# Kernel tuning notes

Measured on AMD Instinct MI355X. Metric: run time of the kernel, lower is better.

Reference implementation:

```python
import jax, jax.numpy as jnp
import numpy as np

SIGMA = 1.0
EPSILON = 1.0
MAX_ITER = 10


def pairwise_kernel(x, y, sigma=SIGMA):
    # k = -||x-y||^2 / (2 sigma^2), shape [B, L, K]
    outer = jnp.einsum('bld,bkd->blk', x, y)
    nx = jnp.sum(x * x, axis=2)
    ny = jnp.sum(y * y, axis=2)
    dist = jnp.clip(nx[:, :, None] + ny[:, None, :] - 2.0 * outer, 0.0, None)
    return -dist / (2.0 * sigma ** 2)


def c_transform(potential, log_weight, kernel, epsilon=EPSILON):
    # rho=None => scale=1, lse = -eps * logsumexp(kernel/eps + (pot/eps + log_w))
    s = potential / epsilon + log_weight            # [B, K]
    operand = kernel / epsilon + s[:, None, :]      # [B, L, K]
    return -epsilon * jax.scipy.special.logsumexp(operand, axis=2)


def potentials(kxy, log_a, log_b):
    kyx = jnp.swapaxes(kxy, 1, 2)
    f0 = jnp.zeros_like(log_a)
    g0 = jnp.zeros_like(log_b)

    def step(carry, _):
        f, g = carry
        fn = c_transform(g, log_b, kxy)
        gn = c_transform(f, log_a, kyx)
        return ((fn + f) * 0.5, (gn + g) * 0.5), None

    (f, g), _ = jax.lax.scan(step, (f0, g0), None, length=MAX_ITER)
    return f, g


def sym_potential(x, log_a):
    kxx = pairwise_kernel(x, x)
    f0 = jnp.zeros_like(log_a)

    def step(f, _):
        fn = c_transform(f, log_a, kxx)
        return (fn + f) * 0.5, None

    f, _ = jax.lax.scan(step, f0, None, length=MAX_ITER)
    return f


def evaluate_potential(x, a, y, b, g):
    # phi_transform is identity for rho=None; scaled_dot_prod forward = sum(a*f, dim=1)
    kxy = pairwise_kernel(x, y)
    f = c_transform(g, jnp.log(b), kxy)
    return jnp.sum(a * f, axis=1)


def setup_inputs() -> dict:
    key = jax.random.key(0)
    k1, k2, k3, k4 = jax.random.split(key, 4)
    B, L, K, D = 8, 2048, 2048, 32
    x = jax.random.normal(k1, (B, L, D), dtype=jnp.float32)
    y = jax.random.normal(k2, (B, K, D), dtype=jnp.float32)
    a = jax.random.uniform(k3, (B, L), dtype=jnp.float32, minval=0.1, maxval=1.0)
    b = jax.random.uniform(k4, (B, K), dtype=jnp.float32, minval=0.1, maxval=1.0)
    a = a / jnp.sum(a, axis=1, keepdims=True)
    b = b / jnp.sum(b, axis=1, keepdims=True)
    return {"x": x, "a": a, "y": y, "b": b}


def reference(x, a, y, b):
    log_a, log_b = jnp.log(a), jnp.log(b)
    kxy = pairwise_kernel(x, y)
    f, g = potentials(kxy, log_a, log_b)
    dist = evaluate_potential(x, a, y, b, g) + evaluate_potential(y, b, x, a, f)
    fx = sym_potential(x, log_a)
    fy = sym_potential(y, log_b)
    ent_x = evaluate_potential(x, a, x, a, fx)
    ent_y = evaluate_potential(y, b, y, b, fy)
    return jnp.mean(dist - ent_x - ent_y)
```

## Files before the change

### kernel.cpp

```cpp
#include <hip/hip_runtime.h>
#include <math.h>

#define BATCH 8
#define NPT   2048
#define DIM   32
#define RPB   64
#define STRIPS (RPB / 16)
#define NBLKR (NPT / RPB)
#define CPW   (NPT / 4)
#define NT    (CPW / 16)
#define L2E   1.44269504088896f
#define LN2   0.6931471805599453f
#define BN    (BATCH * NPT)

typedef __attribute__((ext_vector_type(8))) _Float16 half8;
typedef __attribute__((ext_vector_type(4))) float floatx4;
typedef unsigned short u16;
typedef unsigned int u32;

__device__ __forceinline__ u16 f2h_bits(float v) {
    _Float16 h = (_Float16)v;
    return *(u16*)&h;
}
__device__ __forceinline__ float exp2v(float x) { return __builtin_amdgcn_exp2f(x); }

struct SymSet {
    const u16* Ah;
    const u16* Bh;
    const float* tls;
    const float* qX;
    const float* bmIn;
    const float* cwNext;
    const float* prev;
    float* out;
    float* tlsOut;
    float* bmOut;
};
struct FusedSet {
    const u16* Xh;
    const u16* Ysh;
    const float* tlsG;
    const float* tlsF;
    const float* qX;
    const float* bmG;
    const float* bmF;
    const float* c_x;
    const float* prevF;
    float* outF;
    float* tlsFOut;
    float* bmFOut;
    float* gpart;
};
struct CtArgs { FusedSet fs; SymSet s[2]; int average; };

__global__ __launch_bounds__(256, 3) void ct2_kernel(CtArgs args) {
    const int batch = blockIdx.z;
    const int row0 = blockIdx.x * RPB;
    const int tid  = threadIdx.x;
    const int w = tid >> 6, lane = tid & 63, n = lane & 15, quad = lane >> 4;
    const int qk = quad * 8;
    const size_t pbase = (size_t)batch * NPT * DIM;
    const size_t vbase = (size_t)batch * NPT;

    __shared__ float lsum[RPB][4];

    if (blockIdx.y == 0) {
        const FusedSet fs = args.fs;
        const u16* __restrict__ Ah = fs.Xh + pbase;
        const u16* __restrict__ Bh = fs.Ysh + pbase;
        const float* __restrict__ tg = fs.tlsG + vbase;
        const float* __restrict__ tf = fs.tlsF + vbase;

        half8 ah[STRIPS];
        #pragma unroll
        for (int s = 0; s < STRIPS; s++) {
            size_t off = (size_t)(row0 + s * 16 + n) * DIM + qk;
            ah[s] = *(const half8*)(Ah + off);
        }

        float mg = fmaxf(fs.bmG[batch * 128 + lane], fs.bmG[batch * 128 + 64 + lane]);
        float mf = fmaxf(fs.bmF[batch * 128 + lane], fs.bmF[batch * 128 + 64 + lane]);
        #pragma unroll
        for (int m = 1; m < 64; m <<= 1) {
            mg = fmaxf(mg, __shfl_xor(mg, m, 64));
            mf = fmaxf(mf, __shfl_xor(mf, m, 64));
        }
        const float TmaxG = mg;
        const float l2eTG = L2E * mg, l2eTF = L2E * mf;

        floatx4 cis[STRIPS];
        #pragma unroll
        for (int s = 0; s < STRIPS; s++)
            #pragma unroll
            for (int r = 0; r < 4; r++)
                cis[s][r] = tf[row0 + s * 16 + quad * 4 + r] - l2eTF;

        float sumF[STRIPS][4];
        #pragma unroll
        for (int s = 0; s < STRIPS; s++)
            #pragma unroll
            for (int r = 0; r < 4; r++) sumF[s][r] = 0.0f;

        const int c0 = w * CPW + n;
        const u16* bp = Bh + (size_t)c0 * DIM + qk;
        const float* tp = tg + c0;
        float* gpc = fs.gpart + ((size_t)batch * NBLKR + blockIdx.x) * NPT + c0;

        half8 bb[4];
        float tt[4];
        bb[0] = *(const half8*)bp;                       tt[0] = tp[0];
        bb[1] = *(const half8*)(bp + (size_t)16 * DIM);  tt[1] = tp[16];

        auto tile = [&](half8 b, float t, int idx) {
            float wq = exp2v(t - l2eTG);
            floatx4 acc[STRIPS];
            #pragma unroll
            for (int s = 0; s < STRIPS; s++)
                acc[s] = __builtin_amdgcn_mfma_f32_16x16x32_f16(ah[s], b, cis[s], 0, 0, 0);
            float gl = 0.0f;
            #pragma unroll
            for (int s = 0; s < STRIPS; s++)
                #pragma unroll
                for (int r = 0; r < 4; r++) {
                    float e = exp2v(acc[s][r]);
                    sumF[s][r] = fmaf(wq, e, sumF[s][r]);
                    gl += e;
                }
            gl += __shfl_xor(gl, 16, 64);
            gl += __shfl_xor(gl, 32, 64);
            if (lane < 16) gpc[idx * 16] = gl;
        };

        #pragma unroll 1
        for (int ch = 0; ch < NT; ch += 4) {
            #pragma unroll
            for (int j = 0; j < 4; j++) {
                int nx = ch + j + 2;
                int nxc = nx < NT ? nx : NT - 1;
                bb[(j + 2) & 3] = *(const half8*)(bp + (size_t)nxc * 16 * DIM);
                tt[(j + 2) & 3] = tp[nxc * 16];
                tile(bb[j], tt[j], ch + j);
            }
        }

        #pragma unroll
        for (int s = 0; s < STRIPS; s++)
            #pragma unroll
            for (int r = 0; r < 4; r++) {
                float v = sumF[s][r];
                #pragma unroll
                for (int m = 1; m < 16; m <<= 1) v += __shfl_xor(v, m, 64);
                if (n == 0) lsum[s * 16 + quad * 4 + r][w] = v;
            }
        __syncthreads();

        if (tid < RPB) {
            float T = (lsum[tid][0] + lsum[tid][1]) + (lsum[tid][2] + lsum[tid][3]);
            int l = row0 + tid;
            float lse = TmaxG + __logf(T) - LN2 * (tf[l] - l2eTF);
            float val = fs.qX[vbase + l] - lse;
            if (args.average) val = 0.5f * (fs.prevF[vbase + l] + val);
            fs.outF[vbase + l] = val;
            float tc = val + fs.c_x[vbase + l];
            fs.tlsFOut[vbase + l] = L2E * tc;
            float bm = tc;
            #pragma unroll
            for (int m = 1; m < 16; m <<= 1) bm = fmaxf(bm, __shfl_xor(bm, m, 64));
            if ((tid & 15) == 0)
                fs.bmFOut[batch * 128 + blockIdx.x * STRIPS + (tid >> 4)] = bm;
        }
    } else {
        const SymSet cs = args.s[blockIdx.y - 1];
        const u16* __restrict__ Ah = cs.Ah + pbase;
        const u16* __restrict__ Bh = cs.Bh + pbase;
        const float* __restrict__ tls = cs.tls + vbase;

        half8 ah[STRIPS];
        #pragma unroll
        for (int s = 0; s < STRIPS; s++) {
            size_t off = (size_t)(row0 + s * 16 + n) * DIM + qk;
            ah[s] = *(const half8*)(Ah + off);
        }

        float tmv = fmaxf(cs.bmIn[batch * 128 + lane], cs.bmIn[batch * 128 + 64 + lane]);
        #pragma unroll
        for (int m = 1; m < 64; m <<= 1) tmv = fmaxf(tmv, __shfl_xor(tmv, m, 64));
        const float Tmax = tmv;
        const float l2eTmax = L2E * Tmax;

        float sum[STRIPS][4];
        #pragma unroll
        for (int s = 0; s < STRIPS; s++)
            #pragma unroll
            for (int r = 0; r < 4; r++) sum[s][r] = 0.0f;

        const int c0 = w * CPW + n;
        const u16* bp = Bh + (size_t)c0 * DIM + qk;
        const float* tp = tls + c0;

        half8 bb[4];
        float tt[4];
        bb[0] = *(const half8*)bp;                       tt[0] = tp[0];
        bb[1] = *(const half8*)(bp + (size_t)16 * DIM);  tt[1] = tp[16];

        auto tile = [&](half8 b, float t) {
            float bias = t - l2eTmax;
            floatx4 ci = (floatx4){bias, bias, bias, bias};
            floatx4 acc[STRIPS];
            #pragma unroll
            for (int s = 0; s < STRIPS; s++)
                acc[s] = __builtin_amdgcn_mfma_f32_16x16x32_f16(ah[s], b, ci, 0, 0, 0);
            #pragma unroll
            for (int s = 0; s < STRIPS; s++)
                #pragma unroll
                for (int r = 0; r < 4; r++)
                    sum[s][r] += exp2v(acc[s][r]);
        };

        #pragma unroll 1
        for (int ch = 0; ch < NT; ch += 4) {
            #pragma unroll
            for (int j = 0; j < 4; j++) {
                int nx = ch + j + 2;
                int nxc = nx < NT ? nx : NT - 1;
                bb[(j + 2) & 3] = *(const half8*)(bp + (size_t)nxc * 16 * DIM);
                tt[(j + 2) & 3] = tp[nxc * 16];
                tile(bb[j], tt[j]);
            }
        }

        #pragma unroll
        for (int s = 0; s < STRIPS; s++)
            #pragma unroll
            for (int r = 0; r < 4; r++) {
                float v = sum[s][r];
                #pragma unroll
                for (int m = 1; m < 16; m <<= 1) v += __shfl_xor(v, m, 64);
                if (n == 0) lsum[s * 16 + quad * 4 + r][w] = v;
            }
        __syncthreads();

        if (tid < RPB) {
            float T = (lsum[tid][0] + lsum[tid][1]) + (lsum[tid][2] + lsum[tid][3]);
            int l = row0 + tid;
            float lse = Tmax + __logf(T);
            float val = cs.qX[vbase + l] - lse;
            if (args.average) val = 0.5f * (cs.prev[vbase + l] + val);
            cs.out[vbase + l] = val;
            float tc = val + cs.cwNext[vbase + l];
            cs.tlsOut[vbase + l] = L2E * tc;
            float bm = tc;
            #pragma unroll
            for (int m = 1; m < 16; m <<= 1) bm = fmaxf(bm, __shfl_xor(bm, m, 64));
            if ((tid & 15) == 0)
                cs.bmOut[batch * 128 + blockIdx.x * STRIPS + (tid >> 4)] = bm;
        }
    }
}

struct GfArgs {
    const float* gpart;
    const float* bmF;
    const float* qY;
    const float* prevG;
    const float* c_y;
    float* outG;
    float* tlsGOut;
    float* bmGOut;
    int average;
};

__global__ __launch_bounds__(256) void gfin_kernel(GfArgs a) {
    const int tid = threadIdx.x;
    const int batch = blockIdx.x >> 5;
    const int chunk = blockIdx.x & 31;
    const int g = tid >> 6, c = tid & 63;
    const int col = chunk * 64 + c;

    __shared__ float sb[128];
    __shared__ float ps[4][64];
    if (tid < 128) sb[tid] = a.bmF[batch * 128 + tid];
    __syncthreads();

    float m = fmaxf(sb[tid & 63], sb[(tid & 63) + 64]);
    #pragma unroll
    for (int k = 1; k < 64; k <<= 1) m = fmaxf(m, __shfl_xor(m, k, 64));
    const float Tmax = m;

    const float* gp = a.gpart + ((size_t)batch * NBLKR + g) * NPT + col;
    float G = 0.0f;
    #pragma unroll
    for (int p = 0; p < NBLKR / 4; p++) G += gp[(size_t)p * 4 * NPT];
    ps[g][c] = G;
    __syncthreads();

    if (tid < 64) {
        float Gt = (ps[0][tid] + ps[1][tid]) + (ps[2][tid] + ps[3][tid]);
        const int colT = chunk * 64 + tid;
        const size_t idx = (size_t)batch * NPT + colT;
        float val = a.qY[idx] - (Tmax + __logf(Gt));
        if (a.average) val = 0.5f * (a.prevG[idx] + val);
        a.outG[idx] = val;
        float tc = val + a.c_y[idx];
        a.tlsGOut[idx] = L2E * tc;
        float bm = tc;
        #pragma unroll
        for (int k = 1; k < 16; k <<= 1) bm = fmaxf(bm, __shfl_xor(bm, k, 64));
        if ((tid & 15) == 0) a.bmGOut[batch * 128 + (colT >> 4)] = bm;
    }
}

struct InitArgs {
    const float *x, *a, *y, *b;
    float *c_x, *c_y, *qx, *qy;
    u16 *xh, *yh, *xsh, *ysh;
    float *f0, *g0, *fx0, *fy0;
    float *tlsF0, *tlsG0, *tlsFx0, *tlsFy0;
    float *bmF0, *bmG0, *bmFx0, *bmFy0;
};

__global__ __launch_bounds__(256) void init_kernel(InitArgs ia) {
    int idx = blockIdx.x * 256 + threadIdx.x;
    if (idx >= BN) return;
    const float* xp = ia.x + (size_t)idx * DIM;
    const float* yp = ia.y + (size_t)idx * DIM;
    u32* xhp  = (u32*)ia.xh  + (size_t)idx * (DIM / 2);
    u32* yhp  = (u32*)ia.yh  + (size_t)idx * (DIM / 2);
    u32* xshp = (u32*)ia.xsh + (size_t)idx * (DIM / 2);
    u32* yshp = (u32*)ia.ysh + (size_t)idx * (DIM / 2);
    float sx = 0.f, sy = 0.f;
    #pragma unroll
    for (int d = 0; d < DIM; d += 2) {
        float v0 = xp[d], v1 = xp[d + 1];
        sx += v0 * v0 + v1 * v1;
        xhp[d / 2]  = (u32)f2h_bits(v0) | ((u32)f2h_bits(v1) << 16);
        xshp[d / 2] = (u32)f2h_bits(L2E * v0) | ((u32)f2h_bits(L2E * v1) << 16);
        float u0 = yp[d], u1 = yp[d + 1];
        sy += u0 * u0 + u1 * u1;
        yhp[d / 2]  = (u32)f2h_bits(u0) | ((u32)f2h_bits(u1) << 16);
        yshp[d / 2] = (u32)f2h_bits(L2E * u0) | ((u32)f2h_bits(L2E * u1) << 16);
    }
    float qxv = 0.5f * sx, qyv = 0.5f * sy;
    ia.qx[idx] = qxv; ia.qy[idx] = qyv;
    float cxv = __logf(ia.a[idx]) - qxv;
    float cyv = __logf(ia.b[idx]) - qyv;
    ia.c_x[idx] = cxv; ia.c_y[idx] = cyv;
    ia.f0[idx] = 0.f; ia.g0[idx] = 0.f; ia.fx0[idx] = 0.f; ia.fy0[idx] = 0.f;
    ia.tlsF0[idx] = L2E * cxv; ia.tlsG0[idx] = L2E * cyv;
    ia.tlsFx0[idx] = L2E * cxv; ia.tlsFy0[idx] = L2E * cyv;
    float mx = cxv, my = cyv;
    #pragma unroll
    for (int m = 1; m < 16; m <<= 1) {
        mx = fmaxf(mx, __shfl_xor(mx, m, 32));
        my = fmaxf(my, __shfl_xor(my, m, 32));
    }
    if ((threadIdx.x & 15) == 0) {
        int g = idx >> 4;
        ia.bmF0[g] = mx; ia.bmFx0[g] = mx;
        ia.bmG0[g] = my; ia.bmFy0[g] = my;
    }
}

__global__ __launch_bounds__(1024) void reduce_kernel(
        const float* __restrict__ a, const float* __restrict__ b,
        const float* __restrict__ ctA, const float* __restrict__ ctB,
        const float* __restrict__ ctX, const float* __restrict__ ctY,
        float* __restrict__ out) {
    float acc = 0.f;
    for (int idx = threadIdx.x; idx < BN; idx += 1024) {
        acc += a[idx] * (ctA[idx] - ctX[idx]) + b[idx] * (ctB[idx] - ctY[idx]);
    }
    #pragma unroll
    for (int off = 32; off > 0; off >>= 1) acc += __shfl_down(acc, off, 64);
    __shared__ float sm[16];
    if ((threadIdx.x & 63) == 0) sm[threadIdx.x >> 6] = acc;
    __syncthreads();
    if (threadIdx.x == 0) {
        float t = 0.f;
        #pragma unroll
        for (int i = 0; i < 16; i++) t += sm[i];
        out[0] = t / (float)BATCH;
    }
}

extern "C" void kernel_launch(void* const* d_in, const int* in_sizes, int n_in,
                              void* d_out, int out_size, void* d_ws, size_t ws_size,
                              hipStream_t stream) {
    const float* x = (const float*)d_in[0];
    const float* a = (const float*)d_in[1];
    const float* y = (const float*)d_in[2];
    const float* b = (const float*)d_in[3];
    float* out = (float*)d_out;

    float* ws = (float*)d_ws;
    float* c_x = ws + 0 * BN;
    float* c_y = ws + 1 * BN;
    float* qx  = ws + 2 * BN;
    float* qy  = ws + 3 * BN;
    float* fb[2]  = { ws + 4 * BN,  ws + 5 * BN };
    float* gb[2]  = { ws + 6 * BN,  ws + 7 * BN };
    float* fxb[2] = { ws + 8 * BN,  ws + 9 * BN };
    float* fyb[2] = { ws + 10 * BN, ws + 11 * BN };
    float* ctA = ws + 12 * BN;
    float* ctB = ws + 13 * BN;
    float* ctX = ws + 14 * BN;
    float* ctY = ws + 15 * BN;
    float* tlsF[2]  = { ws + 16 * BN, ws + 17 * BN };
    float* tlsG[2]  = { ws + 18 * BN, ws + 19 * BN };
    float* tlsFx[2] = { ws + 20 * BN, ws + 21 * BN };
    float* tlsFy[2] = { ws + 22 * BN, ws + 23 * BN };
    float* dummyT = ws + 24 * BN;
    float* small = ws + 25 * BN;
    float* bmF[2]  = { small + 0 * 1024, small + 1 * 1024 };
    float* bmG[2]  = { small + 2 * 1024, small + 3 * 1024 };
    float* bmFx[2] = { small + 4 * 1024, small + 5 * 1024 };
    float* bmFy[2] = { small + 6 * 1024, small + 7 * 1024 };
    float* dummyB = small + 8 * 1024;
    u16* bf = (u16*)(small + 10 * 1024);
    const size_t AS = (size_t)BN * DIM;
    u16* xh  = bf + 0 * AS;
    u16* yh  = bf + 1 * AS;
    u16* xsh = bf + 2 * AS;
    u16* ysh = bf + 3 * AS;
    float* gpart = (float*)(bf + 4 * AS);

    InitArgs ia;
    ia.x = x; ia.a = a; ia.y = y; ia.b = b;
    ia.c_x = c_x; ia.c_y = c_y; ia.qx = qx; ia.qy = qy;
    ia.xh = xh; ia.yh = yh; ia.xsh = xsh; ia.ysh = ysh;
    ia.f0 = fb[0]; ia.g0 = gb[0]; ia.fx0 = fxb[0]; ia.fy0 = fyb[0];
    ia.tlsF0 = tlsF[0]; ia.tlsG0 = tlsG[0]; ia.tlsFx0 = tlsFx[0]; ia.tlsFy0 = tlsFy[0];
    ia.bmF0 = bmF[0]; ia.bmG0 = bmG[0]; ia.bmFx0 = bmFx[0]; ia.bmFy0 = bmFy[0];
    init_kernel<<<BN / 256, 256, 0, stream>>>(ia);

    dim3 grid(NBLKR, 3, BATCH);
    int cur = 0;
    for (int it = 0; it < 10; it++) {
        CtArgs ar;
        ar.average = 1;
        ar.fs = { xh, ysh, tlsG[cur], tlsF[cur], qx, bmG[cur], bmF[cur], c_x,
                  fb[cur], fb[1 - cur], tlsF[1 - cur], bmF[1 - cur], gpart };
        ar.s[0] = { xh, xsh, tlsFx[cur], qx, bmFx[cur], c_x,
                    fxb[cur], fxb[1 - cur], tlsFx[1 - cur], bmFx[1 - cur] };
        ar.s[1] = { yh, ysh, tlsFy[cur], qy, bmFy[cur], c_y,
                    fyb[cur], fyb[1 - cur], tlsFy[1 - cur], bmFy[1 - cur] };
        ct2_kernel<<<grid, 256, 0, stream>>>(ar);

        GfArgs ga = { gpart, bmF[cur], qy, gb[cur], c_y,
                      gb[1 - cur], tlsG[1 - cur], bmG[1 - cur], 1 };
        gfin_kernel<<<256, 256, 0, stream>>>(ga);
        cur ^= 1;
    }

    CtArgs fin;
    fin.average = 0;
    fin.fs = { xh, ysh, tlsG[cur], tlsF[cur], qx, bmG[cur], bmF[cur], c_x,
               fb[cur], ctA, dummyT, dummyB, gpart };
    fin.s[0] = { xh, xsh, tlsFx[cur], qx, bmFx[cur], c_x, fxb[cur], ctX, dummyT, dummyB };
    fin.s[1] = { yh, ysh, tlsFy[cur], qy, bmFy[cur], c_y, fyb[cur], ctY, dummyT, dummyB };
    ct2_kernel<<<grid, 256, 0, stream>>>(fin);

    GfArgs gf = { gpart, bmF[cur], qy, gb[cur], c_y, ctB, dummyT, dummyB, 0 };
    gfin_kernel<<<256, 256, 0, stream>>>(gf);

    reduce_kernel<<<1, 1024, 0, stream>>>(a, b, ctA, ctB, ctX, ctY, out);
}
```

Before: 325.0 us.

## Halve rows per block, double occupancy, and shorten B-operand prefetch pipeline

Rows per block drop from 64 to 32 (two MFMA strips instead of four) and the launch bound asks for six blocks per CU instead of three, so more waves are resident to hide latency. The 4-deep rotating prefetch buffer becomes a 2-deep ping-pong with a conditional load, which cuts register use. The per-tile column sum becomes an explicit tree add. Halving RPB doubles the number of blocks and the gpart partial rows, and each B tile is reused across fewer rows, so global/L2 traffic for B rises.

```diff
diff --git a/kernel.cpp b/kernel.cpp
--- a/kernel.cpp
+++ b/kernel.cpp
@@ -4,7 +4,7 @@
 #define BATCH 8
 #define NPT   2048
 #define DIM   32
-#define RPB   64
+#define RPB   32
 #define STRIPS (RPB / 16)
 #define NBLKR (NPT / RPB)
 #define CPW   (NPT / 4)
@@ -53,7 +53,7 @@
 };
 struct CtArgs { FusedSet fs; SymSet s[2]; int average; };
 
-__global__ __launch_bounds__(256, 3) void ct2_kernel(CtArgs args) {
+__global__ __launch_bounds__(256, 6) void ct2_kernel(CtArgs args) {
     const int batch = blockIdx.z;
     const int row0 = blockIdx.x * RPB;
     const int tid  = threadIdx.x;
@@ -106,10 +106,9 @@
         const float* tp = tg + c0;
         float* gpc = fs.gpart + ((size_t)batch * NBLKR + blockIdx.x) * NPT + c0;
 
-        half8 bb[4];
-        float tt[4];
-        bb[0] = *(const half8*)bp;                       tt[0] = tp[0];
-        bb[1] = *(const half8*)(bp + (size_t)16 * DIM);  tt[1] = tp[16];
+        half8 b0, b1;
+        float t0, t1;
+        b0 = *(const half8*)bp;  t0 = *tp;
 
         auto tile = [&](half8 b, float t, int idx) {
             float wq = exp2v(t - l2eTG);
@@ -117,30 +116,31 @@
             #pragma unroll
             for (int s = 0; s < STRIPS; s++)
                 acc[s] = __builtin_amdgcn_mfma_f32_16x16x32_f16(ah[s], b, cis[s], 0, 0, 0);
-            float gl = 0.0f;
+            float e[STRIPS][4];
             #pragma unroll
             for (int s = 0; s < STRIPS; s++)
                 #pragma unroll
                 for (int r = 0; r < 4; r++) {
-                    float e = exp2v(acc[s][r]);
-                    sumF[s][r] = fmaf(wq, e, sumF[s][r]);
-                    gl += e;
+                    e[s][r] = exp2v(acc[s][r]);
+                    sumF[s][r] = fmaf(wq, e[s][r], sumF[s][r]);
                 }
+            float gl = ((e[0][0] + e[0][1]) + (e[0][2] + e[0][3]))
+                     + ((e[1][0] + e[1][1]) + (e[1][2] + e[1][3]));
             gl += __shfl_xor(gl, 16, 64);
             gl += __shfl_xor(gl, 32, 64);
             if (lane < 16) gpc[idx * 16] = gl;
         };
 
         #pragma unroll 1
-        for (int ch = 0; ch < NT; ch += 4) {
-            #pragma unroll
-            for (int j = 0; j < 4; j++) {
-                int nx = ch + j + 2;
-                int nxc = nx < NT ? nx : NT - 1;
-                bb[(j + 2) & 3] = *(const half8*)(bp + (size_t)nxc * 16 * DIM);
-                tt[(j + 2) & 3] = tp[nxc * 16];
-                tile(bb[j], tt[j], ch + j);
+        for (int ch = 0; ch < NT; ch += 2) {
+            b1 = *(const half8*)(bp + (size_t)(ch + 1) * 16 * DIM);
+            t1 = tp[(ch + 1) * 16];
+            tile(b0, t0, ch);
+            if (ch + 2 < NT) {
+                b0 = *(const half8*)(bp + (size_t)(ch + 2) * 16 * DIM);
+                t0 = tp[(ch + 2) * 16];
             }
+            tile(b1, t1, ch + 1);
         }
 
         #pragma unroll
@@ -198,10 +198,9 @@
         const u16* bp = Bh + (size_t)c0 * DIM + qk;
         const float* tp = tls + c0;
 
-        half8 bb[4];
-        float tt[4];
-        bb[0] = *(const half8*)bp;                       tt[0] = tp[0];
-        bb[1] = *(const half8*)(bp + (size_t)16 * DIM);  tt[1] = tp[16];
+        half8 b0, b1;
+        float t0, t1;
+        b0 = *(const half8*)bp;  t0 = *tp;
 
         auto tile = [&](half8 b, float t) {
             float bias = t - l2eTmax;
@@ -218,15 +217,15 @@
         };
 
         #pragma unroll 1
-        for (int ch = 0; ch < NT; ch += 4) {
-            #pragma unroll
-            for (int j = 0; j < 4; j++) {
-                int nx = ch + j + 2;
-                int nxc = nx < NT ? nx : NT - 1;
-                bb[(j + 2) & 3] = *(const half8*)(bp + (size_t)nxc * 16 * DIM);
-                tt[(j + 2) & 3] = tp[nxc * 16];
-                tile(bb[j], tt[j]);
+        for (int ch = 0; ch < NT; ch += 2) {
+            b1 = *(const half8*)(bp + (size_t)(ch + 1) * 16 * DIM);
+            t1 = tp[(ch + 1) * 16];
+            tile(b0, t0);
+            if (ch + 2 < NT) {
+                b0 = *(const half8*)(bp + (size_t)(ch + 2) * 16 * DIM);
+                t0 = tp[(ch + 2) * 16];
             }
+            tile(b1, t1);
         }
 
         #pragma unroll
```

Result: slower. 369.0 us (+13.5%).

## Fold g-potential finalization into next c-transform kernel and fuse final reduction

Applied to the files above, without the earlier changes.

Removes the separate gfin kernel per iteration. Each fused c-transform block now reduces the previous iteration's column partial sums itself, computes the averaged g potential, its max and log-weights into shared memory, and then runs the f update. The final g-transform and the scalar reduction are merged into one kernel that uses an atomic add. This cuts about ten kernel launches and the global round trips for tlsG and bmG. In exchange every block redundantly sums 32 partial rows for all 2048 columns, and a double-buffered gpart array plus extra shared memory and syncs are added.

```diff
diff --git a/kernel.cpp b/kernel.cpp
--- a/kernel.cpp
+++ b/kernel.cpp
@@ -39,23 +39,30 @@
 struct FusedSet {
     const u16* Xh;
     const u16* Ysh;
-    const float* tlsG;
     const float* tlsF;
     const float* qX;
-    const float* bmG;
     const float* bmF;
     const float* c_x;
     const float* prevF;
     float* outF;
     float* tlsFOut;
     float* bmFOut;
-    float* gpart;
+    const float* gpIn;
+    float* gpOut;
+    const float* gbIn;
+    float* gbOut;
+    const float* stfIn;
+    float* stfOut;
+    const float* qY;
+    const float* c_y;
+    int first;
 };
 struct CtArgs { FusedSet fs; SymSet s[2]; int average; };
 
-__global__ __launch_bounds__(256, 3) void ct2_kernel(CtArgs args) {
+__global__ __launch_bounds__(256, 3) void ct3_kernel(CtArgs args) {
     const int batch = blockIdx.z;
-    const int row0 = blockIdx.x * RPB;
+    const int xb = blockIdx.x;
+    const int row0 = xb * RPB;
     const int tid  = threadIdx.x;
     const int w = tid >> 6, lane = tid & 63, n = lane & 15, quad = lane >> 4;
     const int qk = quad * 8;
@@ -63,13 +70,56 @@
     const size_t vbase = (size_t)batch * NPT;
 
     __shared__ float lsum[RPB][4];
+    __shared__ float sg[NPT];
 
     if (blockIdx.y == 0) {
         const FusedSet fs = args.fs;
         const u16* __restrict__ Ah = fs.Xh + pbase;
         const u16* __restrict__ Bh = fs.Ysh + pbase;
-        const float* __restrict__ tg = fs.tlsG + vbase;
         const float* __restrict__ tf = fs.tlsF + vbase;
+        const float* __restrict__ qYp = fs.qY + vbase;
+        const float* __restrict__ cyp = fs.c_y + vbase;
+        const float* __restrict__ gbInp = fs.gbIn + vbase;
+        float* gbOutp = fs.gbOut + vbase;
+
+        float tcv[8];
+        float lmax = -1e30f;
+        if (!fs.first) {
+            const float mfPrev = fs.stfIn[0];
+            const float* gpi = fs.gpIn + (size_t)batch * NBLKR * NPT;
+            #pragma unroll
+            for (int j = 0; j < 8; j++) {
+                const int col = tid + j * 256;
+                float G = 0.f;
+                #pragma unroll 8
+                for (int p = 0; p < NBLKR; p++) G += gpi[(size_t)p * NPT + col];
+                float raw = qYp[col] - (mfPrev + __logf(G));
+                float gnew = 0.5f * (gbInp[col] + raw);
+                if (xb == 0) gbOutp[col] = gnew;
+                float tc = gnew + cyp[col];
+                tcv[j] = tc;
+                lmax = fmaxf(lmax, tc);
+            }
+        } else {
+            #pragma unroll
+            for (int j = 0; j < 8; j++) {
+                const int col = tid + j * 256;
+                if (xb == 0) gbOutp[col] = 0.f;
+                float tc = cyp[col];
+                tcv[j] = tc;
+                lmax = fmaxf(lmax, tc);
+            }
+        }
+        #pragma unroll
+        for (int m = 1; m < 64; m <<= 1) lmax = fmaxf(lmax, __shfl_xor(lmax, m, 64));
+        if (lane == 0) lsum[0][w] = lmax;
+        __syncthreads();
+        const float TmaxG = fmaxf(fmaxf(lsum[0][0], lsum[0][1]),
+                                  fmaxf(lsum[0][2], lsum[0][3]));
+        #pragma unroll
+        for (int j = 0; j < 8; j++)
+            sg[tid + j * 256] = L2E * (tcv[j] - TmaxG);
+        __syncthreads();
 
         half8 ah[STRIPS];
         #pragma unroll
@@ -77,16 +127,11 @@
             size_t off = (size_t)(row0 + s * 16 + n) * DIM + qk;
             ah[s] = *(const half8*)(Ah + off);
         }
-
-        float mg = fmaxf(fs.bmG[batch * 128 + lane], fs.bmG[batch * 128 + 64 + lane]);
         float mf = fmaxf(fs.bmF[batch * 128 + lane], fs.bmF[batch * 128 + 64 + lane]);
         #pragma unroll
-        for (int m = 1; m < 64; m <<= 1) {
-            mg = fmaxf(mg, __shfl_xor(mg, m, 64));
-            mf = fmaxf(mf, __shfl_xor(mf, m, 64));
-        }
-        const float TmaxG = mg;
-        const float l2eTG = L2E * mg, l2eTF = L2E * mf;
+        for (int m = 1; m < 64; m <<= 1) mf = fmaxf(mf, __shfl_xor(mf, m, 64));
+        const float l2eTF = L2E * mf;
+        if (xb == 0 && tid == 0) fs.stfOut[0] = mf;
 
         floatx4 cis[STRIPS];
         #pragma unroll
@@ -103,16 +148,14 @@
 
         const int c0 = w * CPW + n;
         const u16* bp = Bh + (size_t)c0 * DIM + qk;
-        const float* tp = tg + c0;
-        float* gpc = fs.gpart + ((size_t)batch * NBLKR + blockIdx.x) * NPT + c0;
+        float* gpc = fs.gpOut + ((size_t)batch * NBLKR + xb) * NPT + c0;
 
         half8 bb[4];
-        float tt[4];
-        bb[0] = *(const half8*)bp;                       tt[0] = tp[0];
-        bb[1] = *(const half8*)(bp + (size_t)16 * DIM);  tt[1] = tp[16];
-
-        auto tile = [&](half8 b, float t, int idx) {
-            float wq = exp2v(t - l2eTG);
+        bb[0] = *(const half8*)bp;
+        bb[1] = *(const half8*)(bp + (size_t)16 * DIM);
+
+        auto tile = [&](half8 b, int idx) {
+            float wq = exp2v(sg[c0 + idx * 16]);
             floatx4 acc[STRIPS];
             #pragma unroll
             for (int s = 0; s < STRIPS; s++)
@@ -138,8 +181,7 @@
                 int nx = ch + j + 2;
                 int nxc = nx < NT ? nx : NT - 1;
                 bb[(j + 2) & 3] = *(const half8*)(bp + (size_t)nxc * 16 * DIM);
-                tt[(j + 2) & 3] = tp[nxc * 16];
-                tile(bb[j], tt[j], ch + j);
+                tile(bb[j], ch + j);
             }
         }
 
@@ -167,7 +209,7 @@
             #pragma unroll
             for (int m = 1; m < 16; m <<= 1) bm = fmaxf(bm, __shfl_xor(bm, m, 64));
             if ((tid & 15) == 0)
-                fs.bmFOut[batch * 128 + blockIdx.x * STRIPS + (tid >> 4)] = bm;
+                fs.bmFOut[batch * 128 + xb * STRIPS + (tid >> 4)] = bm;
         }
     } else {
         const SymSet cs = args.s[blockIdx.y - 1];
@@ -253,41 +295,34 @@
             #pragma unroll
             for (int m = 1; m < 16; m <<= 1) bm = fmaxf(bm, __shfl_xor(bm, m, 64));
             if ((tid & 15) == 0)
-                cs.bmOut[batch * 128 + blockIdx.x * STRIPS + (tid >> 4)] = bm;
+                cs.bmOut[batch * 128 + xb * STRIPS + (tid >> 4)] = bm;
         }
     }
 }
 
-struct GfArgs {
+struct FrArgs {
     const float* gpart;
-    const float* bmF;
+    const float* stf;
     const float* qY;
-    const float* prevG;
-    const float* c_y;
-    float* outG;
-    float* tlsGOut;
-    float* bmGOut;
-    int average;
+    const float* a;
+    const float* b;
+    const float* ctA;
+    const float* ctX;
+    const float* ctY;
+    float* out;
 };
 
-__global__ __launch_bounds__(256) void gfin_kernel(GfArgs a) {
+__global__ __launch_bounds__(256) void finredux_kernel(FrArgs fa) {
     const int tid = threadIdx.x;
     const int batch = blockIdx.x >> 5;
     const int chunk = blockIdx.x & 31;
     const int g = tid >> 6, c = tid & 63;
     const int col = chunk * 64 + c;
 
-    __shared__ float sb[128];
     __shared__ float ps[4][64];
-    if (tid < 128) sb[tid] = a.bmF[batch * 128 + tid];
-    __syncthreads();
-
-    float m = fmaxf(sb[tid & 63], sb[(tid & 63) + 64]);
-    #pragma unroll
-    for (int k = 1; k < 64; k <<= 1) m = fmaxf(m, __shfl_xor(m, k, 64));
-    const float Tmax = m;
-
-    const float* gp = a.gpart + ((size_t)batch * NBLKR + g) * NPT + col;
+    const float mf = fa.stf[0];
+
+    const float* gp = fa.gpart + ((size_t)batch * NBLKR + g) * NPT + col;
     float G = 0.0f;
     #pragma unroll
     for (int p = 0; p < NBLKR / 4; p++) G += gp[(size_t)p * 4 * NPT];
@@ -298,15 +333,12 @@
         float Gt = (ps[0][tid] + ps[1][tid]) + (ps[2][tid] + ps[3][tid]);
         const int colT = chunk * 64 + tid;
         const size_t idx = (size_t)batch * NPT + colT;
-        float val = a.qY[idx] - (Tmax + __logf(Gt));
-        if (a.average) val = 0.5f * (a.prevG[idx] + val);
-        a.outG[idx] = val;
-        float tc = val + a.c_y[idx];
-        a.tlsGOut[idx] = L2E * tc;
-        float bm = tc;
-        #pragma unroll
-        for (int k = 1; k < 16; k <<= 1) bm = fmaxf(bm, __shfl_xor(bm, k, 64));
-        if ((tid & 15) == 0) a.bmGOut[batch * 128 + (colT >> 4)] = bm;
+        float ctB = fa.qY[idx] - (mf + __logf(Gt));
+        float acc = fa.a[idx] * (fa.ctA[idx] - fa.ctX[idx])
+                  + fa.b[idx] * (ctB - fa.ctY[idx]);
+        #pragma unroll
+        for (int off = 32; off > 0; off >>= 1) acc += __shfl_down(acc, off, 64);
+        if (tid == 0) atomicAdd(fa.out, acc * (1.0f / (float)BATCH));
     }
 }
 
@@ -314,14 +346,16 @@
     const float *x, *a, *y, *b;
     float *c_x, *c_y, *qx, *qy;
     u16 *xh, *yh, *xsh, *ysh;
-    float *f0, *g0, *fx0, *fy0;
-    float *tlsF0, *tlsG0, *tlsFx0, *tlsFy0;
-    float *bmF0, *bmG0, *bmFx0, *bmFy0;
+    float *f0, *fx0, *fy0;
+    float *tlsF0, *tlsFx0, *tlsFy0;
+    float *bmF0, *bmFx0, *bmFy0;
+    float *out;
 };
 
 __global__ __launch_bounds__(256) void init_kernel(InitArgs ia) {
     int idx = blockIdx.x * 256 + threadIdx.x;
     if (idx >= BN) return;
+    if (idx == 0) ia.out[0] = 0.f;
     const float* xp = ia.x + (size_t)idx * DIM;
     const float* yp = ia.y + (size_t)idx * DIM;
     u32* xhp  = (u32*)ia.xh  + (size_t)idx * (DIM / 2);
@@ -345,8 +379,8 @@
     float cxv = __logf(ia.a[idx]) - qxv;
     float cyv = __logf(ia.b[idx]) - qyv;
     ia.c_x[idx] = cxv; ia.c_y[idx] = cyv;
-    ia.f0[idx] = 0.f; ia.g0[idx] = 0.f; ia.fx0[idx] = 0.f; ia.fy0[idx] = 0.f;
-    ia.tlsF0[idx] = L2E * cxv; ia.tlsG0[idx] = L2E * cyv;
+    ia.f0[idx] = 0.f; ia.fx0[idx] = 0.f; ia.fy0[idx] = 0.f;
+    ia.tlsF0[idx] = L2E * cxv;
     ia.tlsFx0[idx] = L2E * cxv; ia.tlsFy0[idx] = L2E * cyv;
     float mx = cxv, my = cyv;
     #pragma unroll
@@ -357,29 +391,7 @@
     if ((threadIdx.x & 15) == 0) {
         int g = idx >> 4;
         ia.bmF0[g] = mx; ia.bmFx0[g] = mx;
-        ia.bmG0[g] = my; ia.bmFy0[g] = my;
-    }
-}
-
-__global__ __launch_bounds__(1024) void reduce_kernel(
-        const float* __restrict__ a, const float* __restrict__ b,
-        const float* __restrict__ ctA, const float* __restrict__ ctB,
-        const float* __restrict__ ctX, const float* __restrict__ ctY,
-        float* __restrict__ out) {
-    float acc = 0.f;
-    for (int idx = threadIdx.x; idx < BN; idx += 1024) {
-        acc += a[idx] * (ctA[idx] - ctX[idx]) + b[idx] * (ctB[idx] - ctY[idx]);
-    }
-    #pragma unroll
-    for (int off = 32; off > 0; off >>= 1) acc += __shfl_down(acc, off, 64);
-    __shared__ float sm[16];
-    if ((threadIdx.x & 63) == 0) sm[threadIdx.x >> 6] = acc;
-    __syncthreads();
-    if (threadIdx.x == 0) {
-        float t = 0.f;
-        #pragma unroll
-        for (int i = 0; i < 16; i++) t += sm[i];
-        out[0] = t / (float)BATCH;
+        ia.bmFy0[g] = my;
     }
 }
 
@@ -398,70 +410,70 @@
     float* qx  = ws + 2 * BN;
     float* qy  = ws + 3 * BN;
     float* fb[2]  = { ws + 4 * BN,  ws + 5 * BN };
-    float* gb[2]  = { ws + 6 * BN,  ws + 7 * BN };
+    float* gbb[2] = { ws + 6 * BN,  ws + 7 * BN };
     float* fxb[2] = { ws + 8 * BN,  ws + 9 * BN };
     float* fyb[2] = { ws + 10 * BN, ws + 11 * BN };
     float* ctA = ws + 12 * BN;
-    float* ctB = ws + 13 * BN;
     float* ctX = ws + 14 * BN;
     float* ctY = ws + 15 * BN;
     float* tlsF[2]  = { ws + 16 * BN, ws + 17 * BN };
-    float* tlsG[2]  = { ws + 18 * BN, ws + 19 * BN };
     float* tlsFx[2] = { ws + 20 * BN, ws + 21 * BN };
     float* tlsFy[2] = { ws + 22 * BN, ws + 23 * BN };
     float* dummyT = ws + 24 * BN;
     float* small = ws + 25 * BN;
     float* bmF[2]  = { small + 0 * 1024, small + 1 * 1024 };
-    float* bmG[2]  = { small + 2 * 1024, small + 3 * 1024 };
     float* bmFx[2] = { small + 4 * 1024, small + 5 * 1024 };
     float* bmFy[2] = { small + 6 * 1024, small + 7 * 1024 };
     float* dummyB = small + 8 * 1024;
+    float* stf = small + 9 * 1024;
     u16* bf = (u16*)(small + 10 * 1024);
     const size_t AS = (size_t)BN * DIM;
     u16* xh  = bf + 0 * AS;
     u16* yh  = bf + 1 * AS;
     u16* xsh = bf + 2 * AS;
     u16* ysh = bf + 3 * AS;
-    float* gpart = (float*)(bf + 4 * AS);
+    float* gp[2];
+    gp[0] = (float*)(bf + 4 * AS);
+    gp[1] = gp[0] + (size_t)BATCH * NBLKR * NPT;
 
     InitArgs ia;
     ia.x = x; ia.a = a; ia.y = y; ia.b = b;
     ia.c_x = c_x; ia.c_y = c_y; ia.qx = qx; ia.qy = qy;
     ia.xh = xh; ia.yh = yh; ia.xsh = xsh; ia.ysh = ysh;
-    ia.f0 = fb[0]; ia.g0 = gb[0]; ia.fx0 = fxb[0]; ia.fy0 = fyb[0];
-    ia.tlsF0 = tlsF[0]; ia.tlsG0 = tlsG[0]; ia.tlsFx0 = tlsFx[0]; ia.tlsFy0 = tlsFy[0];
-    ia.bmF0 = bmF[0]; ia.bmG0 = bmG[0]; ia.bmFx0 = bmFx[0]; ia.bmFy0 = bmFy[0];
+    ia.f0 = fb[0]; ia.fx0 = fxb[0]; ia.fy0 = fyb[0];
+    ia.tlsF0 = tlsF[0]; ia.tlsFx0 = tlsFx[0]; ia.tlsFy0 = tlsFy[0];
+    ia.bmF0 = bmF[0]; ia.bmFx0 = bmFx[0]; ia.bmFy0 = bmFy[0];
+    ia.out = out;
     init_kernel<<<BN / 256, 256, 0, stream>>>(ia);
 
     dim3 grid(NBLKR, 3, BATCH);
-    int cur = 0;
-    for (int it = 0; it < 10; it++) {
+    for (int it = 0; it <= 10; it++) {
+        const int cur = it & 1;
+        const int avg = (it < 10);
         CtArgs ar;
-        ar.average = 1;
-        ar.fs = { xh, ysh, tlsG[cur], tlsF[cur], qx, bmG[cur], bmF[cur], c_x,
-                  fb[cur], fb[1 - cur], tlsF[1 - cur], bmF[1 - cur], gpart };
+        ar.average = avg;
+        ar.fs.Xh = xh; ar.fs.Ysh = ysh;
+        ar.fs.tlsF = tlsF[cur]; ar.fs.qX = qx; ar.fs.bmF = bmF[cur];
+        ar.fs.c_x = c_x; ar.fs.prevF = fb[cur];
+        ar.fs.outF   = avg ? fb[cur ^ 1]   : ctA;
+        ar.fs.tlsFOut = avg ? tlsF[cur ^ 1] : dummyT;
+        ar.fs.bmFOut  = avg ? bmF[cur ^ 1]  : dummyB;
+        ar.fs.gpIn = gp[cur]; ar.fs.gpOut = gp[cur ^ 1];
+        ar.fs.gbIn = gbb[cur]; ar.fs.gbOut = gbb[cur ^ 1];
+        ar.fs.stfIn = stf + cur; ar.fs.stfOut = stf + (cur ^ 1);
+        ar.fs.qY = qy; ar.fs.c_y = c_y;
+        ar.fs.first = (it == 0);
         ar.s[0] = { xh, xsh, tlsFx[cur], qx, bmFx[cur], c_x,
-                    fxb[cur], fxb[1 - cur], tlsFx[1 - cur], bmFx[1 - cur] };
+                    fxb[cur], avg ? fxb[cur ^ 1] : ctX,
+                    avg ? tlsFx[cur ^ 1] : dummyT,
+                    avg ? bmFx[cur ^ 1] : dummyB };
         ar.s[1] = { yh, ysh, tlsFy[cur], qy, bmFy[cur], c_y,
-                    fyb[cur], fyb[1 - cur], tlsFy[1 - cur], bmFy[1 - cur] };
-        ct2_kernel<<<grid, 256, 0, stream>>>(ar);
-
-        GfArgs ga = { gpart, bmF[cur], qy, gb[cur], c_y,
-                      gb[1 - cur], tlsG[1 - cur], bmG[1 - cur], 1 };
-        gfin_kernel<<<256, 256, 0, stream>>>(ga);
-        cur ^= 1;
-    }
-
-    CtArgs fin;
-    fin.average = 0;
-    fin.fs = { xh, ysh, tlsG[cur], tlsF[cur], qx, bmG[cur], bmF[cur], c_x,
-               fb[cur], ctA, dummyT, dummyB, gpart };
-    fin.s[0] = { xh, xsh, tlsFx[cur], qx, bmFx[cur], c_x, fxb[cur], ctX, dummyT, dummyB };
-    fin.s[1] = { yh, ysh, tlsFy[cur], qy, bmFy[cur], c_y, fyb[cur], ctY, dummyT, dummyB };
-    ct2_kernel<<<grid, 256, 0, stream>>>(fin);
-
-    GfArgs gf = { gpart, bmF[cur], qy, gb[cur], c_y, ctB, dummyT, dummyB, 0 };
-    gfin_kernel<<<256, 256, 0, stream>>>(gf);
-
-    reduce_kernel<<<1, 1024, 0, stream>>>(a, b, ctA, ctB, ctX, ctY, out);
+                    fyb[cur], avg ? fyb[cur ^ 1] : ctY,
+                    avg ? tlsFy[cur ^ 1] : dummyT,
+                    avg ? bmFy[cur ^ 1] : dummyB };
+        ct3_kernel<<<grid, 256, 0, stream>>>(ar);
+    }
+
+    FrArgs fa = { gp[1], stf + 1, qy, a, b, ctA, ctX, ctY, out };
+    finredux_kernel<<<256, 256, 0, stream>>>(fa);
 }
```

Result: slower. 451.6 us (+39.0%).
